# Kernel optimization log

Measured on AMD Instinct MI355X. Metric: run time of the kernel, lower is better.

## Reference

```python
import jax, jax.numpy as jnp
import numpy as np

B, S, D, H, DH = 2, 2048, 1024, 16, 64
GLOBAL_RATIO = 0.1
LN_EPS = 1e-5


def setup_inputs() -> dict:
    key = jax.random.key(0)
    ks = jax.random.split(key, 8)
    w = lambda k, shape: jax.random.normal(k, shape, jnp.float32) * 0.02
    return {
        'x': jax.random.normal(ks[0], (B, S, D), jnp.float32),
        'Wq': w(ks[1], (D, H * DH)),
        'Wk': w(ks[2], (D, H * DH)),
        'Wv': w(ks[3], (D, H * DH)),
        'Wo': w(ks[4], (H * DH, D)),
        'bo': jnp.zeros((D,), jnp.float32),
        'ln_gamma': jnp.ones((DH,), jnp.float32),
        'ln_beta': jnp.zeros((DH,), jnp.float32),
        'Wg': w(ks[5], (2 * DH, DH)),
        'bg': jnp.zeros((DH,), jnp.float32),
    }


def _layernorm(x, gamma, beta):
    mu = jnp.mean(x, axis=-1, keepdims=True)
    var = jnp.mean(jnp.square(x - mu), axis=-1, keepdims=True)
    return (x - mu) * jax.lax.rsqrt(var + LN_EPS) * gamma + beta


def reference(x, Wq, Wk, Wv, Wo, bo, ln_gamma, ln_beta, Wg, bg):
    b, s, _ = x.shape
    # projections -> [b, h, n, d]
    split = lambda t: t.reshape(b, s, H, DH).transpose(0, 2, 1, 3)
    q = split(x @ Wq)
    k = split(x @ Wk)
    v = split(x @ Wv)
    scale = DH ** -0.5

    # local (full) attention: manual QK^T / softmax / AV
    scores = jnp.einsum('bhnd,bhmd->bhnm', q, k) * scale  # [b,h,s,s]
    attn = jax.nn.softmax(scores, axis=-1)
    local_out = jnp.einsum('bhnm,bhmd->bhnd', attn, v)

    # cross-segment fusion: top-k keys by norm per (b, h)
    num_global = max(1, int(s * GLOBAL_RATIO))
    key_norms = jnp.linalg.norm(k, axis=-1)  # [b,h,s]
    _, top_idx = jax.lax.top_k(key_norms, num_global)  # [b,h,g]
    idx = top_idx[..., None]  # [b,h,g,1]
    global_k = jnp.take_along_axis(k, idx, axis=2)  # [b,h,g,d]
    global_v = jnp.take_along_axis(v, idx, axis=2)
    g_scores = jnp.einsum('bhnd,bhgd->bhng', q, global_k) * scale
    g_attn = jax.nn.softmax(g_scores, axis=-1)
    global_out = jnp.einsum('bhng,bhgd->bhnd', g_attn, global_v)
    global_out = _layernorm(global_out, ln_gamma, ln_beta)

    # learned gate over [local, global]
    cat = jnp.concatenate([local_out, global_out], axis=-1)  # [b,h,s,2d]
    gate = jax.nn.sigmoid(cat @ Wg + bg)
    fused = gate * local_out + (1.0 - gate) * global_out

    out = fused.transpose(0, 2, 1, 3).reshape(b, s, H * DH)  # b h n d -> b n (h d)
    return out @ Wo + bo
```

## Files before the change

kernel.cpp:

```cpp
#include <hip/hip_runtime.h>


constexpr int SEQ    = 2048;
constexpr int DMODEL = 1024;
constexpr int NH     = 16;
constexpr int DHEAD  = 64;
constexpr int BHT    = 32;
constexpr int NG     = 204;
constexpr int NGPAD  = 256;
constexpr float LNEPS = 1e-5f;

typedef __attribute__((ext_vector_type(8))) short short8;
typedef __attribute__((ext_vector_type(4))) short short4v;
typedef __attribute__((ext_vector_type(4))) float f32x4;

__device__ __forceinline__ unsigned short f2bf(float f) {
    unsigned int u = __float_as_uint(f);
    u += 0x7FFFu + ((u >> 16) & 1u);
    return (unsigned short)(u >> 16);
}
__device__ __forceinline__ float bf2f(unsigned short b) {
    return __uint_as_float(((unsigned int)b) << 16);
}

__global__ __launch_bounds__(256)
void prep_k(const float* __restrict__ x,
            const float* __restrict__ Wq, const float* __restrict__ Wv,
            const float* __restrict__ Wo, const float* __restrict__ Wk,
            const float* __restrict__ Wg,
            unsigned short* __restrict__ xh, unsigned short* __restrict__ xl,
            unsigned short* __restrict__ Wqt, unsigned short* __restrict__ Wvt,
            unsigned short* __restrict__ Wot, unsigned short* __restrict__ Wkh,
            unsigned short* __restrict__ Wkl, unsigned short* __restrict__ Wgt)
{
    const int bid = blockIdx.x;
    const int tid = threadIdx.x;

    if (bid < 2048) {
        int i = (bid * 256 + tid) << 3;
        short8 h, l;
#pragma unroll
        for (int j = 0; j < 8; ++j) {
            float v = x[i + j];
            unsigned short hb = f2bf(v);
            h[j] = (short)hb;
            l[j] = (short)f2bf(v - bf2f(hb));
        }
        *(short8*)(xh + i) = h;
        *(short8*)(xl + i) = l;
        return;
    }
    if (bid == 3072) {
#pragma unroll
        for (int i = 0; i < 32; ++i) {
            int o = tid * 32 + i;
            int dg = o >> 7, jj = o & 127;
            Wgt[o] = f2bf(Wg[jj * 64 + dg]);
        }
        return;
    }

    __shared__ float tile[64][68];
    const int sub = bid - 2048;
    const int which = sub >> 8;
    const int b = sub & 255;
    const int n0 = (b & 15) * 64, k0 = (b >> 4) * 64;
    const float* W = (which == 0) ? Wq : (which == 1) ? Wv : (which == 2) ? Wo : Wk;
    const int Kd = DMODEL, Nd = DMODEL;

#pragma unroll
    for (int p = 0; p < 4; ++p) {
        int c = tid + (p << 8);
        int r = c >> 4, c4 = (c & 15) << 2;
        *(float4*)&tile[r][c4] = *(const float4*)(W + (size_t)(k0 + r) * Nd + n0 + c4);
    }
    __syncthreads();
#pragma unroll
    for (int p = 0; p < 4; ++p) {
        int c = tid + (p << 8);
        int n = c >> 4, k4 = (c & 15) << 2;
        if (which < 3) {
            unsigned short* Wt = (which == 0) ? Wqt : (which == 1) ? Wvt : Wot;
            short4v o;
#pragma unroll
            for (int j = 0; j < 4; ++j) o[j] = (short)f2bf(tile[k4 + j][n]);
            *(short4v*)(Wt + (size_t)(n0 + n) * Kd + k0 + k4) = o;
        } else {
            short4v oh, ol;
#pragma unroll
            for (int j = 0; j < 4; ++j) {
                float v = tile[k4 + j][n];
                unsigned short hb = f2bf(v);
                oh[j] = (short)hb;
                ol[j] = (short)f2bf(v - bf2f(hb));
            }
            *(short4v*)(Wkh + (size_t)(n0 + n) * Kd + k0 + k4) = oh;
            *(short4v*)(Wkl + (size_t)(n0 + n) * Kd + k0 + k4) = ol;
        }
    }
}

__global__ __launch_bounds__(512)
void gemm_bf16_k(const unsigned short* __restrict__ A,
                 const unsigned short* __restrict__ Bt,
                 const float* __restrict__ bias,
                 void* __restrict__ outv, void* __restrict__ outv2,
                 unsigned short* __restrict__ vtout,
                 int M, int N, int K, int mode)
{
    __shared__ __align__(16) unsigned short As[128][72];
    __shared__ __align__(16) unsigned short Bs[128][72];
    const int tid = threadIdx.x;
    const int lane = tid & 63, wave = tid >> 6;
    const int quad = lane >> 4, ln = lane & 15;
    const int mh = (wave >> 2) << 6;
    const int nh = (wave & 3) << 5;
    const int m0 = blockIdx.y * 128, n0 = blockIdx.x * 128;

    f32x4 acc[4][2];
#pragma unroll
    for (int i = 0; i < 4; ++i)
#pragma unroll
        for (int j = 0; j < 2; ++j) acc[i][j] = (f32x4){0.f, 0.f, 0.f, 0.f};

    short8 areg[2], breg[2];
#pragma unroll
    for (int p = 0; p < 2; ++p) {
        int c = tid + (p << 9);
        int row = c >> 3, col8 = (c & 7) << 3;
        areg[p] = *(const short8*)(A + (size_t)(m0 + row) * K + col8);
        breg[p] = *(const short8*)(Bt + (size_t)(n0 + row) * K + col8);
    }

    for (int k0 = 0; k0 < K; k0 += 64) {
        __syncthreads();
#pragma unroll
        for (int p = 0; p < 2; ++p) {
            int c = tid + (p << 9);
            int row = c >> 3, col8 = (c & 7) << 3;
            *(short8*)&As[row][col8] = areg[p];
            *(short8*)&Bs[row][col8] = breg[p];
        }
        __syncthreads();
        if (k0 + 64 < K) {
#pragma unroll
            for (int p = 0; p < 2; ++p) {
                int c = tid + (p << 9);
                int row = c >> 3, col8 = (c & 7) << 3;
                areg[p] = *(const short8*)(A + (size_t)(m0 + row) * K + k0 + 64 + col8);
                breg[p] = *(const short8*)(Bt + (size_t)(n0 + row) * K + k0 + 64 + col8);
            }
        }
#pragma unroll
        for (int ch = 0; ch < 2; ++ch) {
            short8 af[4], bf[2];
#pragma unroll
            for (int mt = 0; mt < 4; ++mt)
                af[mt] = *(const short8*)&As[mh + mt * 16 + ln][ch * 32 + quad * 8];
#pragma unroll
            for (int nt = 0; nt < 2; ++nt)
                bf[nt] = *(const short8*)&Bs[nh + nt * 16 + ln][ch * 32 + quad * 8];
#pragma unroll
            for (int mt = 0; mt < 4; ++mt)
#pragma unroll
                for (int nt = 0; nt < 2; ++nt)
                    acc[mt][nt] = __builtin_amdgcn_mfma_f32_16x16x32_bf16(
                        af[mt], bf[nt], acc[mt][nt], 0, 0, 0);
        }
    }

    if (mode == 0) {
        float* out = (float*)outv;
#pragma unroll
        for (int mt = 0; mt < 4; ++mt)
#pragma unroll
            for (int nt = 0; nt < 2; ++nt)
#pragma unroll
                for (int r = 0; r < 4; ++r) {
                    int m = m0 + mh + mt * 16 + quad * 4 + r;
                    int n = n0 + nh + nt * 16 + ln;
                    out[(size_t)m * N + n] = acc[mt][nt][r] + bias[n];
                }
    } else {
#pragma unroll
        for (int mt = 0; mt < 4; ++mt)
#pragma unroll
            for (int nt = 0; nt < 2; ++nt) {
                int n = n0 + nh + nt * 16 + ln;
                int mb = m0 + mh + mt * 16 + quad * 4;
                int b = mb >> 11, s0 = mb & (SEQ - 1);
                int d = n & 63;
                if (n < DMODEL) {
                    int h = n >> 6;
                    unsigned short* qp_ =
                        (unsigned short*)outv + ((size_t)(b * NH + h) * SEQ + s0) * DHEAD + d;
#pragma unroll
                    for (int r = 0; r < 4; ++r)
                        qp_[(size_t)r * DHEAD] = f2bf(acc[mt][nt][r] * 0.125f);
                } else {
                    int h = (n >> 6) - NH;
                    unsigned short* vp_ =
                        (unsigned short*)outv2 + ((size_t)(b * NH + h) * SEQ + s0) * DHEAD + d;
                    short4v tv;
#pragma unroll
                    for (int r = 0; r < 4; ++r) {
                        unsigned short bv = f2bf(acc[mt][nt][r]);
                        vp_[(size_t)r * DHEAD] = bv;
                        tv[r] = (short)bv;
                    }
                    *(short4v*)(vtout + ((size_t)(b * NH + h) * DHEAD + d) * SEQ + s0) = tv;
                }
            }
    }
}

__global__ __launch_bounds__(512)
void gemm_kproj_mfma(const unsigned short* __restrict__ xh,
                     const unsigned short* __restrict__ xl,
                     const unsigned short* __restrict__ Wh,
                     const unsigned short* __restrict__ Wl,
                     unsigned short* __restrict__ kout,
                     float* __restrict__ norms2)
{
    __shared__ __align__(16) unsigned short Ah[64][72];
    __shared__ __align__(16) unsigned short Al[64][72];
    __shared__ __align__(16) unsigned short Bh[128][72];
    __shared__ __align__(16) unsigned short Bl[128][72];
    const int K = DMODEL;
    const int tid = threadIdx.x;
    const int lane = tid & 63, wave = tid >> 6;
    const int quad = lane >> 4, ln = lane & 15;
    const int mh = (wave >> 1) << 4;
    const int nh = (wave & 1) << 6;
    const int m0 = blockIdx.y * 64, n0 = blockIdx.x * 128;

    f32x4 acc[4];
#pragma unroll
    for (int j = 0; j < 4; ++j) acc[j] = (f32x4){0.f, 0.f, 0.f, 0.f};

    const int arow = tid >> 3, acol8 = (tid & 7) << 3;
    short8 ahreg, alreg, bhreg[2], blreg[2];
    {
        size_t ga = (size_t)(m0 + arow) * K + acol8;
        ahreg = *(const short8*)(xh + ga);
        alreg = *(const short8*)(xl + ga);
#pragma unroll
        for (int p = 0; p < 2; ++p) {
            int c = tid + (p << 9);
            int row = c >> 3, col8 = (c & 7) << 3;
            size_t gb = (size_t)(n0 + row) * K + col8;
            bhreg[p] = *(const short8*)(Wh + gb);
            blreg[p] = *(const short8*)(Wl + gb);
        }
    }

    for (int k0 = 0; k0 < K; k0 += 64) {
        __syncthreads();
        *(short8*)&Ah[arow][acol8] = ahreg;
        *(short8*)&Al[arow][acol8] = alreg;
#pragma unroll
        for (int p = 0; p < 2; ++p) {
            int c = tid + (p << 9);
            int row = c >> 3, col8 = (c & 7) << 3;
            *(short8*)&Bh[row][col8] = bhreg[p];
            *(short8*)&Bl[row][col8] = blreg[p];
        }
        __syncthreads();
        if (k0 + 64 < K) {
            size_t ga = (size_t)(m0 + arow) * K + k0 + 64 + acol8;
            ahreg = *(const short8*)(xh + ga);
            alreg = *(const short8*)(xl + ga);
#pragma unroll
            for (int p = 0; p < 2; ++p) {
                int c = tid + (p << 9);
                int row = c >> 3, col8 = (c & 7) << 3;
                size_t gb = (size_t)(n0 + row) * K + k0 + 64 + col8;
                bhreg[p] = *(const short8*)(Wh + gb);
                blreg[p] = *(const short8*)(Wl + gb);
            }
        }
#pragma unroll
        for (int ch = 0; ch < 2; ++ch) {
            short8 bh4[4], bl4[4];
#pragma unroll
            for (int nt = 0; nt < 4; ++nt) {
                bh4[nt] = *(const short8*)&Bh[nh + nt * 16 + ln][ch * 32 + quad * 8];
                bl4[nt] = *(const short8*)&Bl[nh + nt * 16 + ln][ch * 32 + quad * 8];
            }
            short8 ah = *(const short8*)&Ah[mh + ln][ch * 32 + quad * 8];
            short8 al = *(const short8*)&Al[mh + ln][ch * 32 + quad * 8];
#pragma unroll
            for (int nt = 0; nt < 4; ++nt) {
                acc[nt] = __builtin_amdgcn_mfma_f32_16x16x32_bf16(ah, bh4[nt], acc[nt], 0, 0, 0);
                acc[nt] = __builtin_amdgcn_mfma_f32_16x16x32_bf16(ah, bl4[nt], acc[nt], 0, 0, 0);
                acc[nt] = __builtin_amdgcn_mfma_f32_16x16x32_bf16(al, bh4[nt], acc[nt], 0, 0, 0);
            }
        }
    }

    const int h = (n0 + nh) >> 6;
#pragma unroll
    for (int r = 0; r < 4; ++r) {
        int m = m0 + mh + quad * 4 + r;
        int b = m >> 11, s = m & (SEQ - 1);
        size_t rowbase = ((size_t)(b * NH + h) * SEQ + s) * DHEAD;
#pragma unroll
        for (int nt = 0; nt < 4; ++nt)
            kout[rowbase + nt * 16 + ln] = f2bf(acc[nt][r]);
        float s2 = acc[0][r] * acc[0][r] + acc[1][r] * acc[1][r] +
                   acc[2][r] * acc[2][r] + acc[3][r] * acc[3][r];
#pragma unroll
        for (int off = 1; off <= 8; off <<= 1)
            s2 += __shfl_xor(s2, off);
        if (ln == 0)
            norms2[(size_t)(b * NH + h) * SEQ + s] = s2;
    }
}

__global__ __launch_bounds__(512)
void topk_gather_k(const float* __restrict__ norms2,
                   const unsigned short* __restrict__ k,
                   const unsigned short* __restrict__ v,
                   unsigned short* __restrict__ gk,
                   unsigned short* __restrict__ gvt)
{
    __shared__ unsigned long long keys[SEQ];
    __shared__ int tix[NGPAD];
    __shared__ __align__(16) unsigned short T[64][72];
    const int bh = blockIdx.x;
    const int tid = threadIdx.x;
    const float* nb = norms2 + (size_t)bh * SEQ;
    const size_t base = (size_t)bh * SEQ * DHEAD;

    for (int i = tid; i < SEQ; i += 512) {
        float nrm = sqrtf(nb[i]);
        keys[i] = ((unsigned long long)__float_as_uint(nrm) << 32) |
                  (unsigned int)(0xFFFFFFFFu - (unsigned int)i);
    }
    __syncthreads();
    for (int kk = 2; kk <= SEQ; kk <<= 1) {
        for (int j = kk >> 1; j > 0; j >>= 1) {
            for (int i = tid; i < SEQ; i += 512) {
                int ixj = i ^ j;
                if (ixj > i) {
                    unsigned long long a = keys[i], b = keys[ixj];
                    bool up = ((i & kk) == 0);
                    if ((a > b) == up) { keys[i] = b; keys[ixj] = a; }
                }
            }
            __syncthreads();
        }
    }
    if (tid < NGPAD) {
        tix[tid] = (tid < NG)
            ? (int)(0xFFFFFFFFu - (unsigned int)(keys[SEQ - 1 - tid] & 0xFFFFFFFFu))
            : 0;
    }
    __syncthreads();

    for (int t = 0; t < NGPAD / 64; ++t) {
        {
            int idx = tid;
            int row = idx >> 3, col8 = (idx & 7) << 3;
            int g = t * 64 + row;
            short8 kv = (short8)0, vv = (short8)0;
            if (g < NG) {
                int sidx = tix[g];
                kv = *(const short8*)(k + base + (size_t)sidx * DHEAD + col8);
                vv = *(const short8*)(v + base + (size_t)sidx * DHEAD + col8);
            }
            *(short8*)(gk + ((size_t)bh * NGPAD + g) * DHEAD + col8) = kv;
            *(short8*)&T[row][col8] = vv;
        }
        __syncthreads();
        {
            int idx = tid;
            int d = idx >> 3, k8 = (idx & 7) << 3;
            short8 o;
#pragma unroll
            for (int i = 0; i < 8; ++i) o[i] = (short)T[k8 + i][d];
            *(short8*)(gvt + ((size_t)bh * DHEAD + d) * NGPAD + t * 64 + k8) = o;
        }
        __syncthreads();
    }
}

__global__ __launch_bounds__(256)
void attn_fused_k(const unsigned short* __restrict__ qb,
                  const unsigned short* __restrict__ kb,
                  const unsigned short* __restrict__ vt,
                  const unsigned short* __restrict__ gk,
                  const unsigned short* __restrict__ gvt,
                  const unsigned short* __restrict__ Wgt,
                  const float* __restrict__ gamma,
                  const float* __restrict__ beta,
                  const float* __restrict__ bg,
                  unsigned short* __restrict__ fused)
{
    __shared__ __align__(16) unsigned short KVU[9216];
    __shared__ __align__(16) unsigned short Ps[128][72];
    unsigned short (*Ks)[72] = (unsigned short (*)[72])KVU;
    unsigned short (*Vt)[72] = (unsigned short (*)[72])(KVU + 4608);
    unsigned short (*Wgs)[136] = (unsigned short (*)[136])KVU;

    const int flat = blockIdx.x;
    const int bh = ((flat >> 7) << 3) | (flat & 7);
    const int q0 = ((flat >> 3) & 15) * 128;
    const int tid = threadIdx.x;
    const int lane = tid & 63, wave = tid >> 6;
    const int quad = lane >> 4, ln = lane & 15;
    const size_t base = (size_t)bh * SEQ * DHEAD;
    const unsigned short* gkb = gk + (size_t)bh * NGPAD * DHEAD;
    const unsigned short* gvb = gvt + (size_t)bh * DHEAD * NGPAD;

    short8 qf[2][2];
#pragma unroll
    for (int g = 0; g < 2; ++g) {
        const unsigned short* qp =
            qb + base + (size_t)(q0 + wave * 32 + g * 16 + ln) * DHEAD;
        qf[g][0] = *(const short8*)(qp + quad * 8);
        qf[g][1] = *(const short8*)(qp + 32 + quad * 8);
    }

    f32x4 O[2][4], Og[2][4];
#pragma unroll
    for (int g = 0; g < 2; ++g)
#pragma unroll
        for (int nt = 0; nt < 4; ++nt) {
            O[g][nt] = (f32x4){0.f, 0.f, 0.f, 0.f};
            Og[g][nt] = (f32x4){0.f, 0.f, 0.f, 0.f};
        }
    float ls[2][4] = {{0.f, 0.f, 0.f, 0.f}, {0.f, 0.f, 0.f, 0.f}};
    float lg[2][4] = {{0.f, 0.f, 0.f, 0.f}, {0.f, 0.f, 0.f, 0.f}};

    short8 kreg[2], vreg[2];
#pragma unroll
    for (int p = 0; p < 2; ++p) {
        int idx = tid * 2 + p;
        int row = idx >> 3, col8 = (idx & 7) << 3;
        kreg[p] = *(const short8*)(kb + base + (size_t)row * DHEAD + col8);
        vreg[p] = *(const short8*)(vt + base + (size_t)row * SEQ + col8);
    }

    const int NT_LOCAL = SEQ / 64, NT_GLOB = NGPAD / 64;
    for (int t = 0; t < NT_LOCAL + NT_GLOB; ++t) {
        const bool isglob = (t >= NT_LOCAL);
        __syncthreads();
#pragma unroll
        for (int p = 0; p < 2; ++p) {
            int idx = tid * 2 + p;
            int row = idx >> 3, col8 = (idx & 7) << 3;
            *(short8*)&Ks[row][col8] = kreg[p];
            *(short8*)&Vt[row][col8] = vreg[p];
        }
        __syncthreads();
        if (t + 1 < NT_LOCAL) {
#pragma unroll
            for (int p = 0; p < 2; ++p) {
                int idx = tid * 2 + p;
                int row = idx >> 3, col8 = (idx & 7) << 3;
                kreg[p] = *(const short8*)(kb + base + (size_t)((t + 1) * 64 + row) * DHEAD + col8);
                vreg[p] = *(const short8*)(vt + base + (size_t)row * SEQ + (t + 1) * 64 + col8);
            }
        } else if (t + 1 < NT_LOCAL + NT_GLOB) {
            int tg = t + 1 - NT_LOCAL;
#pragma unroll
            for (int p = 0; p < 2; ++p) {
                int idx = tid * 2 + p;
                int row = idx >> 3, col8 = (idx & 7) << 3;
                kreg[p] = *(const short8*)(gkb + (size_t)(tg * 64 + row) * DHEAD + col8);
                vreg[p] = *(const short8*)(gvb + (size_t)row * NGPAD + tg * 64 + col8);
            }
        }

        short8 kf0[4], kf1[4];
#pragma unroll
        for (int nt = 0; nt < 4; ++nt) {
            kf0[nt] = *(const short8*)&Ks[nt * 16 + ln][quad * 8];
            kf1[nt] = *(const short8*)&Ks[nt * 16 + ln][32 + quad * 8];
        }
#pragma unroll
        for (int g = 0; g < 2; ++g) {
            f32x4 s[4];
#pragma unroll
            for (int nt = 0; nt < 4; ++nt) {
                s[nt] = (f32x4){0.f, 0.f, 0.f, 0.f};
                s[nt] = __builtin_amdgcn_mfma_f32_16x16x32_bf16(qf[g][0], kf0[nt], s[nt], 0, 0, 0);
                s[nt] = __builtin_amdgcn_mfma_f32_16x16x32_bf16(qf[g][1], kf1[nt], s[nt], 0, 0, 0);
            }
            if (!isglob) {
#pragma unroll
                for (int nt = 0; nt < 4; ++nt)
#pragma unroll
                    for (int r = 0; r < 4; ++r) {
                        float p = __expf(s[nt][r]);
                        unsigned int us = __float_as_uint(p) >> 16;
                        Ps[wave * 32 + g * 16 + quad * 4 + r][nt * 16 + ln] = (unsigned short)us;
                        ls[g][r] += __uint_as_float(us << 16);
                    }
            } else {
                int tg64 = (t - NT_LOCAL) * 64;
#pragma unroll
                for (int nt = 0; nt < 4; ++nt) {
                    bool valid = (tg64 + nt * 16 + ln) < NG;
#pragma unroll
                    for (int r = 0; r < 4; ++r) {
                        float p = valid ? __expf(s[nt][r]) : 0.f;
                        unsigned int us = __float_as_uint(p) >> 16;
                        Ps[wave * 32 + g * 16 + quad * 4 + r][nt * 16 + ln] = (unsigned short)us;
                        lg[g][r] += __uint_as_float(us << 16);
                    }
                }
            }
        }

        short8 vf[4];
#pragma unroll
        for (int ch = 0; ch < 2; ++ch) {
#pragma unroll
            for (int nt = 0; nt < 4; ++nt)
                vf[nt] = *(const short8*)&Vt[nt * 16 + ln][ch * 32 + quad * 8];
#pragma unroll
            for (int g = 0; g < 2; ++g) {
                short8 pf = *(const short8*)&Ps[wave * 32 + g * 16 + ln][ch * 32 + quad * 8];
#pragma unroll
                for (int nt = 0; nt < 4; ++nt) {
                    if (!isglob)
                        O[g][nt] = __builtin_amdgcn_mfma_f32_16x16x32_bf16(pf, vf[nt], O[g][nt], 0, 0, 0);
                    else
                        Og[g][nt] = __builtin_amdgcn_mfma_f32_16x16x32_bf16(pf, vf[nt], Og[g][nt], 0, 0, 0);
                }
            }
        }
    }

    __syncthreads();
#pragma unroll
    for (int p = 0; p < 4; ++p) {
        int idx8 = tid + (p << 8);
        int dg = idx8 >> 4, c8 = (idx8 & 15) << 3;
        *(short8*)&Wgs[dg][c8] = *(const short8*)(Wgt + idx8 * 8);
    }
    __syncthreads();

#pragma unroll
    for (int off = 1; off <= 8; off <<= 1)
#pragma unroll
        for (int g = 0; g < 2; ++g)
#pragma unroll
            for (int r = 0; r < 4; ++r) {
                ls[g][r] += __shfl_xor(ls[g][r], off);
                lg[g][r] += __shfl_xor(lg[g][r], off);
            }

    const int b = bh >> 4, h = bh & 15;
#pragma unroll
    for (int g = 0; g < 2; ++g) {
        float xs[4][4];
#pragma unroll
        for (int r = 0; r < 4; ++r) {
            float inv = 1.f / lg[g][r];
#pragma unroll
            for (int nt = 0; nt < 4; ++nt) xs[nt][r] = Og[g][nt][r] * inv;
        }
        float mu[4], rsd[4];
#pragma unroll
        for (int r = 0; r < 4; ++r) {
            float sm = xs[0][r] + xs[1][r] + xs[2][r] + xs[3][r];
#pragma unroll
            for (int off = 1; off <= 8; off <<= 1) sm += __shfl_xor(sm, off);
            mu[r] = sm * (1.f / 64.f);
        }
#pragma unroll
        for (int r = 0; r < 4; ++r) {
            float sv = 0.f;
#pragma unroll
            for (int nt = 0; nt < 4; ++nt) {
                float d = xs[nt][r] - mu[r];
                sv += d * d;
            }
#pragma unroll
            for (int off = 1; off <= 8; off <<= 1) sv += __shfl_xor(sv, off);
            rsd[r] = rsqrtf(sv * (1.f / 64.f) + LNEPS);
        }
#pragma unroll
        for (int nt = 0; nt < 4; ++nt) {
            float gmv = gamma[nt * 16 + ln], bb = beta[nt * 16 + ln];
#pragma unroll
            for (int r = 0; r < 4; ++r)
                xs[nt][r] = (xs[nt][r] - mu[r]) * rsd[r] * gmv + bb;
        }

        float lf[4][4];
#pragma unroll
        for (int nt = 0; nt < 4; ++nt)
#pragma unroll
            for (int r = 0; r < 4; ++r) {
                lf[nt][r] = O[g][nt][r] / ls[g][r];
                Ps[wave * 32 + g * 16 + quad * 4 + r][nt * 16 + ln] = f2bf(lf[nt][r]);
            }
        f32x4 gacc[4];
#pragma unroll
        for (int ng = 0; ng < 4; ++ng) {
            float bgv = bg[ng * 16 + ln];
            gacc[ng] = (f32x4){bgv, bgv, bgv, bgv};
        }
#pragma unroll
        for (int ch = 0; ch < 2; ++ch) {
            short8 af = *(const short8*)&Ps[wave * 32 + g * 16 + ln][ch * 32 + quad * 8];
#pragma unroll
            for (int ng = 0; ng < 4; ++ng) {
                short8 bf = *(const short8*)&Wgs[ng * 16 + ln][ch * 32 + quad * 8];
                gacc[ng] = __builtin_amdgcn_mfma_f32_16x16x32_bf16(af, bf, gacc[ng], 0, 0, 0);
            }
        }
#pragma unroll
        for (int nt = 0; nt < 4; ++nt)
#pragma unroll
            for (int r = 0; r < 4; ++r)
                Ps[wave * 32 + g * 16 + quad * 4 + r][nt * 16 + ln] = f2bf(xs[nt][r]);
#pragma unroll
        for (int ch = 0; ch < 2; ++ch) {
            short8 af = *(const short8*)&Ps[wave * 32 + g * 16 + ln][ch * 32 + quad * 8];
#pragma unroll
            for (int ng = 0; ng < 4; ++ng) {
                short8 bf = *(const short8*)&Wgs[ng * 16 + ln][64 + ch * 32 + quad * 8];
                gacc[ng] = __builtin_amdgcn_mfma_f32_16x16x32_bf16(af, bf, gacc[ng], 0, 0, 0);
            }
        }

#pragma unroll
        for (int ng = 0; ng < 4; ++ng)
#pragma unroll
            for (int r = 0; r < 4; ++r) {
                float gt = 1.f / (1.f + __expf(-gacc[ng][r]));
                float f = gt * lf[ng][r] + (1.f - gt) * xs[ng][r];
                int s = q0 + wave * 32 + g * 16 + quad * 4 + r;
                fused[((size_t)(b * SEQ + s)) * DMODEL + h * DHEAD + ng * 16 + ln] = f2bf(f);
            }
    }
}

extern "C" void kernel_launch(void* const* d_in, const int* in_sizes, int n_in,
                              void* d_out, int out_size, void* d_ws, size_t ws_size,
                              hipStream_t stream)
{
    (void)in_sizes; (void)n_in; (void)out_size; (void)ws_size;
    const float* x    = (const float*)d_in[0];
    const float* Wq   = (const float*)d_in[1];
    const float* Wk   = (const float*)d_in[2];
    const float* Wv   = (const float*)d_in[3];
    const float* Wo   = (const float*)d_in[4];
    const float* bo   = (const float*)d_in[5];
    const float* ln_g = (const float*)d_in[6];
    const float* ln_b = (const float*)d_in[7];
    const float* Wg   = (const float*)d_in[8];
    const float* bg   = (const float*)d_in[9];

    char* w = (char*)d_ws;
    const size_t MB = 1024ull * 1024ull;
    unsigned short* kb16  = (unsigned short*)(w);
    unsigned short* qb16  = (unsigned short*)(w + 8 * MB);
    unsigned short* vb16  = (unsigned short*)(w + 16 * MB);
    unsigned short* vt16  = (unsigned short*)(w + 24 * MB);
    unsigned short* xh    = (unsigned short*)(w + 32 * MB);
    unsigned short* xl    = (unsigned short*)(w + 40 * MB);
    unsigned short* Wqt   = (unsigned short*)(w + 48 * MB);
    unsigned short* Wvt   = (unsigned short*)(w + 50 * MB);
    unsigned short* Wot   = (unsigned short*)(w + 52 * MB);
    unsigned short* Wkh   = (unsigned short*)(w + 54 * MB);
    unsigned short* Wkl   = (unsigned short*)(w + 56 * MB);
    unsigned short* Wgt   = (unsigned short*)(w + 58 * MB);
    float*          norms2= (float*)(w + 59 * MB);
    unsigned short* gk16  = (unsigned short*)(w + 60 * MB);
    unsigned short* gvt16 = (unsigned short*)(w + 61 * MB);
    unsigned short* fusedb = xh;

    const int M = 4096, N = 1024, K = 1024;

    prep_k<<<3073, 256, 0, stream>>>(x, Wq, Wv, Wo, Wk, Wg,
                                     xh, xl, Wqt, Wvt, Wot, Wkh, Wkl, Wgt);

    dim3 gqv(2048 / 128, M / 128);
    gemm_bf16_k<<<gqv, 512, 0, stream>>>(xh, Wqt, nullptr, qb16, vb16, vt16,
                                         M, 2048, K, 3);

    dim3 gkp(N / 128, M / 64);
    gemm_kproj_mfma<<<gkp, 512, 0, stream>>>(xh, xl, Wkh, Wkl, kb16, norms2);

    topk_gather_k<<<BHT, 512, 0, stream>>>(norms2, kb16, vb16, gk16, gvt16);

    attn_fused_k<<<512, 256, 0, stream>>>(qb16, kb16, vt16, gk16, gvt16, Wgt,
                                          ln_g, ln_b, bg, fusedb);

    dim3 go_(N / 128, M / 128);
    gemm_bf16_k<<<go_, 512, 0, stream>>>(fusedb, Wot, bo, (float*)d_out, nullptr,
                                         nullptr, M, N, K, 0);
}
```

Baseline: 301.8 us.

## Split KV tiles across two wave groups in fused attention and merge partials

```diff
diff --git a/kernel.cpp b/kernel.cpp
--- a/kernel.cpp
+++ b/kernel.cpp
@@ -385,7 +385,7 @@
     }
 }
 
-__global__ __launch_bounds__(256)
+__global__ __launch_bounds__(512, 4)
 void attn_fused_k(const unsigned short* __restrict__ qb,
                   const unsigned short* __restrict__ kb,
                   const unsigned short* __restrict__ vt,
@@ -397,27 +397,30 @@
                   const float* __restrict__ bg,
                   unsigned short* __restrict__ fused)
 {
-    __shared__ __align__(16) unsigned short KVU[9216];
-    __shared__ __align__(16) unsigned short Ps[128][72];
-    unsigned short (*Ks)[72] = (unsigned short (*)[72])KVU;
-    unsigned short (*Vt)[72] = (unsigned short (*)[72])(KVU + 4608);
-    unsigned short (*Wgs)[136] = (unsigned short (*)[136])KVU;
+    __shared__ __align__(16) unsigned short Ks[2][64][72];
+    __shared__ __align__(16) unsigned short Vt[2][64][72];
+    __shared__ __align__(16) unsigned short Ps[256][40];
+    unsigned short (*Wgs)[136] = (unsigned short (*)[136])&Ks[0][0][0];
+    float* scrO = (float*)&Ps[0][0];
+    float* scr3 = (float*)&Vt[0][0][0];
 
     const int flat = blockIdx.x;
     const int bh = ((flat >> 7) << 3) | (flat & 7);
     const int q0 = ((flat >> 3) & 15) * 128;
     const int tid = threadIdx.x;
     const int lane = tid & 63, wave = tid >> 6;
+    const int grp = wave >> 2, wg = wave & 3;
     const int quad = lane >> 4, ln = lane & 15;
     const size_t base = (size_t)bh * SEQ * DHEAD;
     const unsigned short* gkb = gk + (size_t)bh * NGPAD * DHEAD;
     const unsigned short* gvb = gvt + (size_t)bh * DHEAD * NGPAD;
+    const int tid256 = tid & 255;
 
     short8 qf[2][2];
 #pragma unroll
     for (int g = 0; g < 2; ++g) {
         const unsigned short* qp =
-            qb + base + (size_t)(q0 + wave * 32 + g * 16 + ln) * DHEAD;
+            qb + base + (size_t)(q0 + wg * 32 + g * 16 + ln) * DHEAD;
         qf[g][0] = *(const short8*)(qp + quad * 8);
         qf[g][1] = *(const short8*)(qp + 32 + quad * 8);
     }
@@ -436,99 +439,104 @@
     short8 kreg[2], vreg[2];
 #pragma unroll
     for (int p = 0; p < 2; ++p) {
-        int idx = tid * 2 + p;
+        int idx = tid256 * 2 + p;
         int row = idx >> 3, col8 = (idx & 7) << 3;
-        kreg[p] = *(const short8*)(kb + base + (size_t)row * DHEAD + col8);
-        vreg[p] = *(const short8*)(vt + base + (size_t)row * SEQ + col8);
-    }
-
-    const int NT_LOCAL = SEQ / 64, NT_GLOB = NGPAD / 64;
-    for (int t = 0; t < NT_LOCAL + NT_GLOB; ++t) {
-        const bool isglob = (t >= NT_LOCAL);
+        kreg[p] = *(const short8*)(kb + base + (size_t)(grp * 64 + row) * DHEAD + col8);
+        vreg[p] = *(const short8*)(vt + base + (size_t)row * SEQ + grp * 64 + col8);
+    }
+
+    for (int it = 0; it < 18; ++it) {
+        const int mytile = 2 * it + grp;
+        const bool isglob = (mytile >= 32);
+        const int tg64 = (mytile - 32) * 64;
         __syncthreads();
 #pragma unroll
         for (int p = 0; p < 2; ++p) {
-            int idx = tid * 2 + p;
+            int idx = tid256 * 2 + p;
             int row = idx >> 3, col8 = (idx & 7) << 3;
-            *(short8*)&Ks[row][col8] = kreg[p];
-            *(short8*)&Vt[row][col8] = vreg[p];
+            *(short8*)&Ks[grp][row][col8] = kreg[p];
+            *(short8*)&Vt[grp][row][col8] = vreg[p];
         }
         __syncthreads();
-        if (t + 1 < NT_LOCAL) {
-#pragma unroll
-            for (int p = 0; p < 2; ++p) {
-                int idx = tid * 2 + p;
-                int row = idx >> 3, col8 = (idx & 7) << 3;
-                kreg[p] = *(const short8*)(kb + base + (size_t)((t + 1) * 64 + row) * DHEAD + col8);
-                vreg[p] = *(const short8*)(vt + base + (size_t)row * SEQ + (t + 1) * 64 + col8);
-            }
-        } else if (t + 1 < NT_LOCAL + NT_GLOB) {
-            int tg = t + 1 - NT_LOCAL;
-#pragma unroll
-            for (int p = 0; p < 2; ++p) {
-                int idx = tid * 2 + p;
-                int row = idx >> 3, col8 = (idx & 7) << 3;
-                kreg[p] = *(const short8*)(gkb + (size_t)(tg * 64 + row) * DHEAD + col8);
-                vreg[p] = *(const short8*)(gvb + (size_t)row * NGPAD + tg * 64 + col8);
-            }
-        }
-
-        short8 kf0[4], kf1[4];
-#pragma unroll
-        for (int nt = 0; nt < 4; ++nt) {
-            kf0[nt] = *(const short8*)&Ks[nt * 16 + ln][quad * 8];
-            kf1[nt] = *(const short8*)&Ks[nt * 16 + ln][32 + quad * 8];
-        }
-#pragma unroll
-        for (int g = 0; g < 2; ++g) {
-            f32x4 s[4];
-#pragma unroll
-            for (int nt = 0; nt < 4; ++nt) {
-                s[nt] = (f32x4){0.f, 0.f, 0.f, 0.f};
-                s[nt] = __builtin_amdgcn_mfma_f32_16x16x32_bf16(qf[g][0], kf0[nt], s[nt], 0, 0, 0);
-                s[nt] = __builtin_amdgcn_mfma_f32_16x16x32_bf16(qf[g][1], kf1[nt], s[nt], 0, 0, 0);
-            }
-            if (!isglob) {
-#pragma unroll
-                for (int nt = 0; nt < 4; ++nt)
-#pragma unroll
-                    for (int r = 0; r < 4; ++r) {
-                        float p = __expf(s[nt][r]);
-                        unsigned int us = __float_as_uint(p) >> 16;
-                        Ps[wave * 32 + g * 16 + quad * 4 + r][nt * 16 + ln] = (unsigned short)us;
-                        ls[g][r] += __uint_as_float(us << 16);
-                    }
-            } else {
-                int tg64 = (t - NT_LOCAL) * 64;
-#pragma unroll
-                for (int nt = 0; nt < 4; ++nt) {
-                    bool valid = (tg64 + nt * 16 + ln) < NG;
-#pragma unroll
-                    for (int r = 0; r < 4; ++r) {
-                        float p = valid ? __expf(s[nt][r]) : 0.f;
-                        unsigned int us = __float_as_uint(p) >> 16;
-                        Ps[wave * 32 + g * 16 + quad * 4 + r][nt * 16 + ln] = (unsigned short)us;
-                        lg[g][r] += __uint_as_float(us << 16);
+        {
+            int nxt = mytile + 2;
+            if (nxt < 32) {
+#pragma unroll
+                for (int p = 0; p < 2; ++p) {
+                    int idx = tid256 * 2 + p;
+                    int row = idx >> 3, col8 = (idx & 7) << 3;
+                    kreg[p] = *(const short8*)(kb + base + (size_t)(nxt * 64 + row) * DHEAD + col8);
+                    vreg[p] = *(const short8*)(vt + base + (size_t)row * SEQ + nxt * 64 + col8);
+                }
+            } else if (nxt < 36) {
+                int tg = nxt - 32;
+#pragma unroll
+                for (int p = 0; p < 2; ++p) {
+                    int idx = tid256 * 2 + p;
+                    int row = idx >> 3, col8 = (idx & 7) << 3;
+                    kreg[p] = *(const short8*)(gkb + (size_t)(tg * 64 + row) * DHEAD + col8);
+                    vreg[p] = *(const short8*)(gvb + (size_t)row * NGPAD + tg * 64 + col8);
+                }
+            }
+        }
+
+#pragma unroll
+        for (int ch = 0; ch < 2; ++ch) {
+            short8 kf0[2], kf1[2];
+#pragma unroll
+            for (int j = 0; j < 2; ++j) {
+                int ntj = ch * 2 + j;
+                kf0[j] = *(const short8*)&Ks[grp][ntj * 16 + ln][quad * 8];
+                kf1[j] = *(const short8*)&Ks[grp][ntj * 16 + ln][32 + quad * 8];
+            }
+#pragma unroll
+            for (int g = 0; g < 2; ++g) {
+                f32x4 s[2];
+#pragma unroll
+                for (int j = 0; j < 2; ++j) {
+                    s[j] = (f32x4){0.f, 0.f, 0.f, 0.f};
+                    s[j] = __builtin_amdgcn_mfma_f32_16x16x32_bf16(qf[g][0], kf0[j], s[j], 0, 0, 0);
+                    s[j] = __builtin_amdgcn_mfma_f32_16x16x32_bf16(qf[g][1], kf1[j], s[j], 0, 0, 0);
+                }
+                if (!isglob) {
+#pragma unroll
+                    for (int j = 0; j < 2; ++j)
+#pragma unroll
+                        for (int r = 0; r < 4; ++r) {
+                            float p = __expf(s[j][r]);
+                            unsigned int us = __float_as_uint(p) >> 16;
+                            Ps[wave * 32 + g * 16 + quad * 4 + r][j * 16 + ln] = (unsigned short)us;
+                            ls[g][r] += __uint_as_float(us << 16);
+                        }
+                } else {
+#pragma unroll
+                    for (int j = 0; j < 2; ++j) {
+                        bool valid = (tg64 + (ch * 2 + j) * 16 + ln) < NG;
+#pragma unroll
+                        for (int r = 0; r < 4; ++r) {
+                            float p = valid ? __expf(s[j][r]) : 0.f;
+                            unsigned int us = __float_as_uint(p) >> 16;
+                            Ps[wave * 32 + g * 16 + quad * 4 + r][j * 16 + ln] = (unsigned short)us;
+                            lg[g][r] += __uint_as_float(us << 16);
+                        }
                     }
                 }
             }
-        }
-
-        short8 vf[4];
-#pragma unroll
-        for (int ch = 0; ch < 2; ++ch) {
-#pragma unroll
-            for (int nt = 0; nt < 4; ++nt)
-                vf[nt] = *(const short8*)&Vt[nt * 16 + ln][ch * 32 + quad * 8];
+            short8 vf[4];
+#pragma unroll
+            for (int ntp = 0; ntp < 4; ++ntp)
+                vf[ntp] = *(const short8*)&Vt[grp][ntp * 16 + ln][ch * 32 + quad * 8];
 #pragma unroll
             for (int g = 0; g < 2; ++g) {
-                short8 pf = *(const short8*)&Ps[wave * 32 + g * 16 + ln][ch * 32 + quad * 8];
-#pragma unroll
-                for (int nt = 0; nt < 4; ++nt) {
-                    if (!isglob)
-                        O[g][nt] = __builtin_amdgcn_mfma_f32_16x16x32_bf16(pf, vf[nt], O[g][nt], 0, 0, 0);
-                    else
-                        Og[g][nt] = __builtin_amdgcn_mfma_f32_16x16x32_bf16(pf, vf[nt], Og[g][nt], 0, 0, 0);
+                short8 pf = *(const short8*)&Ps[wave * 32 + g * 16 + ln][quad * 8];
+                if (!isglob) {
+#pragma unroll
+                    for (int ntp = 0; ntp < 4; ++ntp)
+                        O[g][ntp] = __builtin_amdgcn_mfma_f32_16x16x32_bf16(pf, vf[ntp], O[g][ntp], 0, 0, 0);
+                } else {
+#pragma unroll
+                    for (int ntp = 0; ntp < 4; ++ntp)
+                        Og[g][ntp] = __builtin_amdgcn_mfma_f32_16x16x32_bf16(pf, vf[ntp], Og[g][ntp], 0, 0, 0);
                 }
             }
         }
@@ -536,13 +544,11 @@
 
     __syncthreads();
 #pragma unroll
-    for (int p = 0; p < 4; ++p) {
-        int idx8 = tid + (p << 8);
+    for (int p = 0; p < 2; ++p) {
+        int idx8 = tid * 2 + p;
         int dg = idx8 >> 4, c8 = (idx8 & 15) << 3;
         *(short8*)&Wgs[dg][c8] = *(const short8*)(Wgt + idx8 * 8);
     }
-    __syncthreads();
-
 #pragma unroll
     for (int off = 1; off <= 8; off <<= 1)
 #pragma unroll
@@ -552,93 +558,160 @@
                 ls[g][r] += __shfl_xor(ls[g][r], off);
                 lg[g][r] += __shfl_xor(lg[g][r], off);
             }
+    {
+        int og = grp ^ 1;
+#pragma unroll
+        for (int r = 0; r < 4; ++r) {
+            scr3[((size_t)wave * 64 + lane) * 8 + r] = ls[og][r];
+            scr3[((size_t)wave * 64 + lane) * 8 + 4 + r] = lg[og][r];
+        }
+    }
+    const int slot = wg * 1024 + lane * 16;
+    if (grp == 0)
+#pragma unroll
+        for (int nt = 0; nt < 4; ++nt)
+#pragma unroll
+            for (int r = 0; r < 4; ++r) scrO[slot + nt * 4 + r] = O[1][nt][r];
+    __syncthreads();
+    if (grp == 1) {
+#pragma unroll
+        for (int nt = 0; nt < 4; ++nt)
+#pragma unroll
+            for (int r = 0; r < 4; ++r) O[1][nt][r] += scrO[slot + nt * 4 + r];
+#pragma unroll
+        for (int nt = 0; nt < 4; ++nt)
+#pragma unroll
+            for (int r = 0; r < 4; ++r) scrO[slot + nt * 4 + r] = O[0][nt][r];
+    }
+    __syncthreads();
+    if (grp == 0) {
+#pragma unroll
+        for (int nt = 0; nt < 4; ++nt)
+#pragma unroll
+            for (int r = 0; r < 4; ++r) O[0][nt][r] += scrO[slot + nt * 4 + r];
+#pragma unroll
+        for (int nt = 0; nt < 4; ++nt)
+#pragma unroll
+            for (int r = 0; r < 4; ++r) scrO[slot + nt * 4 + r] = Og[1][nt][r];
+    }
+    __syncthreads();
+    if (grp == 1) {
+#pragma unroll
+        for (int nt = 0; nt < 4; ++nt)
+#pragma unroll
+            for (int r = 0; r < 4; ++r) Og[1][nt][r] += scrO[slot + nt * 4 + r];
+#pragma unroll
+        for (int nt = 0; nt < 4; ++nt)
+#pragma unroll
+            for (int r = 0; r < 4; ++r) scrO[slot + nt * 4 + r] = Og[0][nt][r];
+    }
+    __syncthreads();
+    if (grp == 0)
+#pragma unroll
+        for (int nt = 0; nt < 4; ++nt)
+#pragma unroll
+            for (int r = 0; r < 4; ++r) Og[0][nt][r] += scrO[slot + nt * 4 + r];
+    float lsum[4], lgsum[4];
+    {
+        int prt = wave ^ 4;
+#pragma unroll
+        for (int r = 0; r < 4; ++r) {
+            lsum[r] = ls[grp][r] + scr3[((size_t)prt * 64 + lane) * 8 + r];
+            lgsum[r] = lg[grp][r] + scr3[((size_t)prt * 64 + lane) * 8 + 4 + r];
+        }
+    }
+    __syncthreads();
+
+    const int myg = grp;
+    float xs[4][4];
+#pragma unroll
+    for (int r = 0; r < 4; ++r) {
+        float inv = 1.f / lgsum[r];
+#pragma unroll
+        for (int nt = 0; nt < 4; ++nt) xs[nt][r] = Og[myg][nt][r] * inv;
+    }
+    float mu[4], rsd[4];
+#pragma unroll
+    for (int r = 0; r < 4; ++r) {
+        float sm = xs[0][r] + xs[1][r] + xs[2][r] + xs[3][r];
+#pragma unroll
+        for (int off = 1; off <= 8; off <<= 1) sm += __shfl_xor(sm, off);
+        mu[r] = sm * (1.f / 64.f);
+    }
+#pragma unroll
+    for (int r = 0; r < 4; ++r) {
+        float sv = 0.f;
+#pragma unroll
+        for (int nt = 0; nt < 4; ++nt) {
+            float d = xs[nt][r] - mu[r];
+            sv += d * d;
+        }
+#pragma unroll
+        for (int off = 1; off <= 8; off <<= 1) sv += __shfl_xor(sv, off);
+        rsd[r] = rsqrtf(sv * (1.f / 64.f) + LNEPS);
+    }
+#pragma unroll
+    for (int nt = 0; nt < 4; ++nt) {
+        float gmv = gamma[nt * 16 + ln], bb = beta[nt * 16 + ln];
+#pragma unroll
+        for (int r = 0; r < 4; ++r)
+            xs[nt][r] = (xs[nt][r] - mu[r]) * rsd[r] * gmv + bb;
+    }
+    float lf[4][4];
+#pragma unroll
+    for (int nt = 0; nt < 4; ++nt)
+#pragma unroll
+        for (int r = 0; r < 4; ++r) lf[nt][r] = O[myg][nt][r] / lsum[r];
+
+    f32x4 gacc[4];
+#pragma unroll
+    for (int ng = 0; ng < 4; ++ng) {
+        float bgv = bg[ng * 16 + ln];
+        gacc[ng] = (f32x4){bgv, bgv, bgv, bgv};
+    }
+#pragma unroll
+    for (int ch = 0; ch < 2; ++ch) {
+#pragma unroll
+        for (int j = 0; j < 2; ++j) {
+            int nt = ch * 2 + j;
+#pragma unroll
+            for (int r = 0; r < 4; ++r)
+                Ps[wave * 32 + quad * 4 + r][j * 16 + ln] = f2bf(lf[nt][r]);
+        }
+        short8 af = *(const short8*)&Ps[wave * 32 + ln][quad * 8];
+#pragma unroll
+        for (int ng = 0; ng < 4; ++ng) {
+            short8 bf = *(const short8*)&Wgs[ng * 16 + ln][ch * 32 + quad * 8];
+            gacc[ng] = __builtin_amdgcn_mfma_f32_16x16x32_bf16(af, bf, gacc[ng], 0, 0, 0);
+        }
+    }
+#pragma unroll
+    for (int ch = 0; ch < 2; ++ch) {
+#pragma unroll
+        for (int j = 0; j < 2; ++j) {
+            int nt = ch * 2 + j;
+#pragma unroll
+            for (int r = 0; r < 4; ++r)
+                Ps[wave * 32 + quad * 4 + r][j * 16 + ln] = f2bf(xs[nt][r]);
+        }
+        short8 af = *(const short8*)&Ps[wave * 32 + ln][quad * 8];
+#pragma unroll
+        for (int ng = 0; ng < 4; ++ng) {
+            short8 bf = *(const short8*)&Wgs[ng * 16 + ln][64 + ch * 32 + quad * 8];
+            gacc[ng] = __builtin_amdgcn_mfma_f32_16x16x32_bf16(af, bf, gacc[ng], 0, 0, 0);
+        }
+    }
 
     const int b = bh >> 4, h = bh & 15;
 #pragma unroll
-    for (int g = 0; g < 2; ++g) {
-        float xs[4][4];
+    for (int ng = 0; ng < 4; ++ng)
 #pragma unroll
         for (int r = 0; r < 4; ++r) {
-            float inv = 1.f / lg[g][r];
-#pragma unroll
-            for (int nt = 0; nt < 4; ++nt) xs[nt][r] = Og[g][nt][r] * inv;
-        }
-        float mu[4], rsd[4];
-#pragma unroll
-        for (int r = 0; r < 4; ++r) {
-            float sm = xs[0][r] + xs[1][r] + xs[2][r] + xs[3][r];
-#pragma unroll
-            for (int off = 1; off <= 8; off <<= 1) sm += __shfl_xor(sm, off);
-            mu[r] = sm * (1.f / 64.f);
-        }
-#pragma unroll
-        for (int r = 0; r < 4; ++r) {
-            float sv = 0.f;
-#pragma unroll
-            for (int nt = 0; nt < 4; ++nt) {
-                float d = xs[nt][r] - mu[r];
-                sv += d * d;
-            }
-#pragma unroll
-            for (int off = 1; off <= 8; off <<= 1) sv += __shfl_xor(sv, off);
-            rsd[r] = rsqrtf(sv * (1.f / 64.f) + LNEPS);
-        }
-#pragma unroll
-        for (int nt = 0; nt < 4; ++nt) {
-            float gmv = gamma[nt * 16 + ln], bb = beta[nt * 16 + ln];
-#pragma unroll
-            for (int r = 0; r < 4; ++r)
-                xs[nt][r] = (xs[nt][r] - mu[r]) * rsd[r] * gmv + bb;
-        }
-
-        float lf[4][4];
-#pragma unroll
-        for (int nt = 0; nt < 4; ++nt)
-#pragma unroll
-            for (int r = 0; r < 4; ++r) {
-                lf[nt][r] = O[g][nt][r] / ls[g][r];
-                Ps[wave * 32 + g * 16 + quad * 4 + r][nt * 16 + ln] = f2bf(lf[nt][r]);
-            }
-        f32x4 gacc[4];
-#pragma unroll
-        for (int ng = 0; ng < 4; ++ng) {
-            float bgv = bg[ng * 16 + ln];
-            gacc[ng] = (f32x4){bgv, bgv, bgv, bgv};
-        }
-#pragma unroll
-        for (int ch = 0; ch < 2; ++ch) {
-            short8 af = *(const short8*)&Ps[wave * 32 + g * 16 + ln][ch * 32 + quad * 8];
-#pragma unroll
-            for (int ng = 0; ng < 4; ++ng) {
-                short8 bf = *(const short8*)&Wgs[ng * 16 + ln][ch * 32 + quad * 8];
-                gacc[ng] = __builtin_amdgcn_mfma_f32_16x16x32_bf16(af, bf, gacc[ng], 0, 0, 0);
-            }
-        }
-#pragma unroll
-        for (int nt = 0; nt < 4; ++nt)
-#pragma unroll
-            for (int r = 0; r < 4; ++r)
-                Ps[wave * 32 + g * 16 + quad * 4 + r][nt * 16 + ln] = f2bf(xs[nt][r]);
-#pragma unroll
-        for (int ch = 0; ch < 2; ++ch) {
-            short8 af = *(const short8*)&Ps[wave * 32 + g * 16 + ln][ch * 32 + quad * 8];
-#pragma unroll
-            for (int ng = 0; ng < 4; ++ng) {
-                short8 bf = *(const short8*)&Wgs[ng * 16 + ln][64 + ch * 32 + quad * 8];
-                gacc[ng] = __builtin_amdgcn_mfma_f32_16x16x32_bf16(af, bf, gacc[ng], 0, 0, 0);
-            }
-        }
-
-#pragma unroll
-        for (int ng = 0; ng < 4; ++ng)
-#pragma unroll
-            for (int r = 0; r < 4; ++r) {
-                float gt = 1.f / (1.f + __expf(-gacc[ng][r]));
-                float f = gt * lf[ng][r] + (1.f - gt) * xs[ng][r];
-                int s = q0 + wave * 32 + g * 16 + quad * 4 + r;
-                fused[((size_t)(b * SEQ + s)) * DMODEL + h * DHEAD + ng * 16 + ln] = f2bf(f);
-            }
-    }
+            float gt = 1.f / (1.f + __expf(-gacc[ng][r]));
+            float f = gt * lf[ng][r] + (1.f - gt) * xs[ng][r];
+            int s = q0 + wg * 32 + myg * 16 + quad * 4 + r;
+            fused[((size_t)(b * SEQ + s)) * DMODEL + h * DHEAD + ng * 16 + ln] = f2bf(f);
+        }
 }
 
 extern "C" void kernel_launch(void* const* d_in, const int* in_sizes, int n_in,
@@ -690,7 +763,7 @@
 
     topk_gather_k<<<BHT, 512, 0, stream>>>(norms2, kb16, vb16, gk16, gvt16);
 
-    attn_fused_k<<<512, 256, 0, stream>>>(qb16, kb16, vt16, gk16, gvt16, Wgt,
+    attn_fused_k<<<512, 512, 0, stream>>>(qb16, kb16, vt16, gk16, gvt16, Wgt,
                                           ln_g, ln_b, bg, fusedb);
 
     dim3 go_(N / 128, M / 128);
```

Measured after the change: 517.5 us. +71.5%, slower.
